# Optimization experiments

Hardware: AMD Instinct MI355X
Metric: run time of the kernel (lower is better)

Reference implementation:

```python
import jax, jax.numpy as jnp
import numpy as np

B, D, E, H, L = 32768, 512, 10, 128, 2  # batch, input_dim, max_charts, expert hidden, latent_dim
RH1, RH2 = 256, 128                      # router hidden sizes
TAU = 3.0


def setup_inputs() -> dict:
    key = jax.random.key(0)
    ks = jax.random.split(key, 16)
    rnd = lambda k, *s: (jax.random.normal(k, s, jnp.float32) * 0.05)
    return {
        "x": jax.random.normal(ks[0], (B, D), jnp.float32),
        "u": jax.random.uniform(ks[1], (B, E), jnp.float32),
        # router params (last layer init ~ N(0, 0.01), bias 0, as in _init_router)
        "rw1": rnd(ks[2], D, RH1), "rb1": jnp.zeros((RH1,), jnp.float32),
        "rw2": rnd(ks[3], RH1, RH2), "rb2": jnp.zeros((RH2,), jnp.float32),
        "rw3": jax.random.normal(ks[4], (RH2, E), jnp.float32) * 0.01,
        "rb3": jnp.zeros((E,), jnp.float32),
        # stacked expert params: all 10 experts batched along leading dim
        "ew1": rnd(ks[5], E, D, H), "eb1": rnd(ks[6], E, H),
        "ew2": rnd(ks[7], E, H, H), "eb2": rnd(ks[8], E, H),
        "ew3": rnd(ks[9], E, H, L), "eb3": rnd(ks[10], E, L),
    }


def reference(x, u, rw1, rb1, rw2, rb2, rw3, rb3, ew1, eb1, ew2, eb2, ew3, eb3):
    # router MLP: D -> 256 -> 128 -> E
    h = jax.nn.relu(x @ rw1 + rb1)
    h = jax.nn.relu(h @ rw2 + rb2)
    logits = h @ rw3 + rb3                                  # [B, E]
    # gumbel_softmax(tau=3.0, hard=False): softmax((logits + gumbel)/tau)
    g = -jnp.log(-jnp.log(jnp.clip(u, 1e-10, 1.0)) + 1e-10)
    weights = jax.nn.softmax((logits + g) / TAU, axis=1)    # [B, E]
    # all 10 experts as batched GEMMs (fuses the python loop over charts)
    h1 = jax.nn.relu(jnp.einsum('bi,eio->beo', x, ew1) + eb1[None])   # [B, E, H]
    h2 = jax.nn.relu(jnp.einsum('beh,eho->beo', h1, ew2) + eb2[None]) # [B, E, H]
    zc = jnp.einsum('beh,ehl->bel', h2, ew3) + eb3[None]              # [B, E, L]
    z = jnp.einsum('be,bel->bl', weights, zc)                         # [B, L]
    chart_outputs = jnp.transpose(zc, (1, 0, 2))                      # [E, B, L]
    return z, weights, chart_outputs
```

## Files before the change

### kernel.cpp

```cpp
#include <hip/hip_runtime.h>
#include <stdint.h>

typedef __bf16 bf16x8 __attribute__((ext_vector_type(8)));
typedef float floatx4 __attribute__((ext_vector_type(4)));
typedef unsigned short ushort_t;

__device__ __forceinline__ ushort_t bf16rne(float f) {
    union { float f; unsigned u; } v; v.f = f;
    return (ushort_t)((v.u + 0x7fffu + ((v.u >> 16) & 1u)) >> 16);
}

__device__ __forceinline__ void gl_lds16(const ushort_t* g, ushort_t* l) {
    __builtin_amdgcn_global_load_lds(
        (const __attribute__((address_space(1))) unsigned int*)g,
        (__attribute__((address_space(3))) unsigned int*)l, 16, 0, 0);
}

__device__ __forceinline__ void transpose_body(const float* __restrict__ in,
                                               ushort_t* __restrict__ outp,
                                               int idx, int K, int N, int total) {
    if (idx >= total) return;
    int kn = K * N;
    int e = idx / kn;
    int r = idx - e * kn;
    int n = r / K;
    int k = r - n * K;
    outp[idx] = bf16rne(in[e * kn + k * N + n]);
}

__global__ void prep(const float* __restrict__ x, ushort_t* __restrict__ x16,
                     const float* __restrict__ ew1, ushort_t* __restrict__ ew1t,
                     const float* __restrict__ ew2, ushort_t* __restrict__ ew2t,
                     const float* __restrict__ rw1, ushort_t* __restrict__ rw1t,
                     const float* __restrict__ rw2, ushort_t* __restrict__ rw2t) {
    int b = blockIdx.x, tid = threadIdx.x;
    if (b < 16384) {
        int i = b * 256 + tid;
        float4 f = ((const float4*)x)[i];
        union { ushort_t s[4]; uint2 v; } pk;
        pk.s[0] = bf16rne(f.x); pk.s[1] = bf16rne(f.y);
        pk.s[2] = bf16rne(f.z); pk.s[3] = bf16rne(f.w);
        ((uint2*)x16)[i] = pk.v;
    } else if (b < 18944) {
        transpose_body(ew1, ew1t, (b - 16384) * 256 + tid, 512, 128, 655360);
    } else if (b < 19584) {
        transpose_body(ew2, ew2t, (b - 18944) * 256 + tid, 128, 128, 163840);
    } else if (b < 20096) {
        transpose_body(rw1, rw1t, (b - 19584) * 256 + tid, 512, 256, 131072);
    } else {
        transpose_body(rw2, rw2t, (b - 20096) * 256 + tid, 256, 128, 32768);
    }
}

__global__ __launch_bounds__(256, 4)
void router_l1(const ushort_t* __restrict__ x16, const ushort_t* __restrict__ rw1t,
               const float* __restrict__ rb1, ushort_t* __restrict__ hr1) {
    __shared__ alignas(16) ushort_t sX[4096];
    __shared__ alignas(16) ushort_t sW[4096];
    __shared__ float sBias[128];

    const int tid = threadIdx.x;
    const int rb = blockIdx.x, nb = blockIdx.y;
    const int wave = tid >> 6, lane = tid & 63;
    const int ln15 = lane & 15, q = lane >> 4;
    const int wm = (wave & 1) * 64, wn = (wave >> 1) * 64;
    const int mhalf = wm >> 6, nhalf = wn >> 6;

    if (tid < 128) sBias[tid] = rb1[nb * 128 + tid];

    const ushort_t* xblk = x16 + (size_t)rb * 128 * 512;
    const ushort_t* wbase = rw1t + (size_t)nb * 128 * 512;

    const int s0 = wave, s1 = wave + 4;
    const int srow0 = (wave * 16) + (lane >> 2);
    const int srow1 = 64 + (wave * 16) + (lane >> 2);
    const int scol = (lane & 3) * 8;

    floatx4 acc[4][4];
#pragma unroll
    for (int i = 0; i < 4; ++i)
#pragma unroll
        for (int j = 0; j < 4; ++j) acc[i][j] = (floatx4){0.f, 0.f, 0.f, 0.f};

    for (int k0 = 0; k0 < 512; k0 += 32) {
        __syncthreads();
        gl_lds16(xblk + (size_t)srow0 * 512 + k0 + scol, &sX[s0 * 512]);
        gl_lds16(xblk + (size_t)srow1 * 512 + k0 + scol, &sX[s1 * 512]);
        gl_lds16(wbase + (size_t)srow0 * 512 + k0 + scol, &sW[s0 * 512]);
        gl_lds16(wbase + (size_t)srow1 * 512 + k0 + scol, &sW[s1 * 512]);
        __syncthreads();
        bf16x8 a[4], b[4];
#pragma unroll
        for (int t = 0; t < 4; ++t) a[t] = *(const bf16x8*)(&sW[(mhalf * 4 + t) * 512 + ln15 * 32 + q * 8]);
#pragma unroll
        for (int t = 0; t < 4; ++t) b[t] = *(const bf16x8*)(&sX[(nhalf * 4 + t) * 512 + ln15 * 32 + q * 8]);
#pragma unroll
        for (int i = 0; i < 4; ++i)
#pragma unroll
            for (int j = 0; j < 4; ++j)
                acc[i][j] = __builtin_amdgcn_mfma_f32_16x16x32_bf16(a[i], b[j], acc[i][j], 0, 0, 0);
    }

    const int rbase = rb * 128;
#pragma unroll
    for (int i = 0; i < 4; ++i) {
        int n0 = wm + i * 16 + q * 4;
#pragma unroll
        for (int j = 0; j < 4; ++j) {
            int row = wn + j * 16 + ln15;
            union { ushort_t s[4]; uint2 v; } pk;
#pragma unroll
            for (int r = 0; r < 4; ++r)
                pk.s[r] = bf16rne(fmaxf(acc[i][j][r] + sBias[n0 + r], 0.f));
            *(uint2*)(&hr1[(size_t)(rbase + row) * 256 + nb * 128 + n0]) = pk.v;
        }
    }
}

__global__ __launch_bounds__(256, 2)
void router2(const ushort_t* __restrict__ hr1, const ushort_t* __restrict__ rw2t,
             const float* __restrict__ rb2, const float* __restrict__ rw3,
             const float* __restrict__ rb3, const float* __restrict__ u,
             float* __restrict__ wts, float* __restrict__ z) {
    __shared__ alignas(16) ushort_t sA[4096];
    __shared__ alignas(16) ushort_t sB[4096];
    __shared__ float sw3[1280];
    __shared__ float sBias[128];
    __shared__ float lgbuf[128][10];

    const int tid = threadIdx.x;
    const int rb = blockIdx.x;
    const int wave = tid >> 6, lane = tid & 63;
    const int ln15 = lane & 15, q = lane >> 4;
    const int wm = (wave & 1) * 64, wn = (wave >> 1) * 64;
    const int mhalf = wm >> 6, nhalf = wn >> 6;

    for (int i = tid; i < 1280; i += 256) sw3[i] = rw3[i];
    if (tid < 128) sBias[tid] = rb2[tid];

    const ushort_t* brow = hr1 + (size_t)rb * 128 * 256;
    const int s0 = wave, s1 = wave + 4;
    const int srow0 = (wave * 16) + (lane >> 2);
    const int srow1 = 64 + (wave * 16) + (lane >> 2);
    const int scol = (lane & 3) * 8;

    floatx4 acc2[4][4];
#pragma unroll
    for (int i = 0; i < 4; ++i)
#pragma unroll
        for (int j = 0; j < 4; ++j) acc2[i][j] = (floatx4){0.f, 0.f, 0.f, 0.f};

    for (int k0 = 0; k0 < 256; k0 += 32) {
        __syncthreads();
        gl_lds16(rw2t + (size_t)srow0 * 256 + k0 + scol, &sA[s0 * 512]);
        gl_lds16(rw2t + (size_t)srow1 * 256 + k0 + scol, &sA[s1 * 512]);
        gl_lds16(brow + (size_t)srow0 * 256 + k0 + scol, &sB[s0 * 512]);
        gl_lds16(brow + (size_t)srow1 * 256 + k0 + scol, &sB[s1 * 512]);
        __syncthreads();
        bf16x8 a[4], b[4];
#pragma unroll
        for (int t = 0; t < 4; ++t) a[t] = *(const bf16x8*)(&sA[(mhalf * 4 + t) * 512 + ln15 * 32 + q * 8]);
#pragma unroll
        for (int t = 0; t < 4; ++t) b[t] = *(const bf16x8*)(&sB[(nhalf * 4 + t) * 512 + ln15 * 32 + q * 8]);
#pragma unroll
        for (int i = 0; i < 4; ++i)
#pragma unroll
            for (int j = 0; j < 4; ++j)
                acc2[i][j] = __builtin_amdgcn_mfma_f32_16x16x32_bf16(a[i], b[j], acc2[i][j], 0, 0, 0);
    }

    float lg[4][10];
#pragma unroll
    for (int j = 0; j < 4; ++j)
#pragma unroll
        for (int ee = 0; ee < 10; ++ee) lg[j][ee] = 0.f;
#pragma unroll
    for (int i = 0; i < 4; ++i) {
#pragma unroll
        for (int r = 0; r < 4; ++r) {
            int n = wm + i * 16 + q * 4 + r;
            float bias = sBias[n];
            const float* w3r = &sw3[n * 10];
#pragma unroll
            for (int j = 0; j < 4; ++j) {
                float val = fmaxf(acc2[i][j][r] + bias, 0.f);
#pragma unroll
                for (int ee = 0; ee < 10; ++ee) lg[j][ee] += val * w3r[ee];
            }
        }
    }
#pragma unroll
    for (int j = 0; j < 4; ++j)
#pragma unroll
        for (int ee = 0; ee < 10; ++ee) {
            lg[j][ee] += __shfl_xor(lg[j][ee], 16, 64);
            lg[j][ee] += __shfl_xor(lg[j][ee], 32, 64);
        }
    if (wm == 0 && q == 0) {
#pragma unroll
        for (int j = 0; j < 4; ++j) {
            int row = wn + 16 * j + ln15;
#pragma unroll
            for (int ee = 0; ee < 10; ++ee) lgbuf[row][ee] = lg[j][ee];
        }
    }
    __syncthreads();
    if (wm == 64 && q == 0) {
#pragma unroll
        for (int j = 0; j < 4; ++j) {
            int row = wn + 16 * j + ln15;
#pragma unroll
            for (int ee = 0; ee < 10; ++ee) lgbuf[row][ee] += lg[j][ee];
        }
    }
    __syncthreads();
    if (tid < 128) {
        int grow = rb * 128 + tid;
        float v[10], mx = -1e30f;
#pragma unroll
        for (int ee = 0; ee < 10; ++ee) {
            float uu = u[(size_t)grow * 10 + ee];
            uu = fminf(fmaxf(uu, 1e-10f), 1.0f);
            float g = -logf(-logf(uu) + 1e-10f);
            v[ee] = (lgbuf[tid][ee] + rb3[ee] + g) * (1.0f / 3.0f);
            mx = fmaxf(mx, v[ee]);
        }
        float s = 0.f;
#pragma unroll
        for (int ee = 0; ee < 10; ++ee) { v[ee] = expf(v[ee] - mx); s += v[ee]; }
        float inv = 1.0f / s;
#pragma unroll
        for (int ee = 0; ee < 10; ++ee) wts[(size_t)grow * 10 + ee] = v[ee] * inv;
    }
    z[rb * 256 + tid] = 0.f;
}

__global__ __launch_bounds__(256, 3)
void expert_fused(const ushort_t* __restrict__ x16, const ushort_t* __restrict__ ew1t,
                  const ushort_t* __restrict__ ew2t, const float* __restrict__ eb1,
                  const float* __restrict__ eb2, const float* __restrict__ ew3,
                  const float* __restrict__ eb3, const float* __restrict__ wts,
                  float* __restrict__ chart, float* __restrict__ z) {
    __shared__ alignas(16) ushort_t sX[4096];
    __shared__ alignas(16) ushort_t sW[4096];
    __shared__ alignas(16) ushort_t sH1[16384];
    __shared__ float sB1[128];
    __shared__ float sB2[128];
    __shared__ float sW3[256];
    __shared__ float zbuf[128][2];

    const int tid = threadIdx.x;
    const int id = blockIdx.x;
    const int xcd = id & 7, local = id >> 3;
    const int e = local % 10;
    const int rb = xcd * 32 + local / 10;

    const int wave = tid >> 6, lane = tid & 63;
    const int ln15 = lane & 15, q = lane >> 4;
    const int wm = (wave & 1) * 64, wn = (wave >> 1) * 64;
    const int mhalf = wm >> 6, nhalf = wn >> 6;

    if (tid < 128) sB1[tid] = eb1[e * 128 + tid];
    else sB2[tid - 128] = eb2[e * 128 + (tid - 128)];
    sW3[tid] = ew3[e * 256 + tid];

    const ushort_t* xblk = x16 + (size_t)rb * 128 * 512;
    const ushort_t* w1 = ew1t + (size_t)e * 128 * 512;
    const ushort_t* w2 = ew2t + (size_t)e * 128 * 128;

    const int s0 = wave, s1 = wave + 4;
    const int srow0 = (wave * 16) + (lane >> 2);
    const int srow1 = 64 + (wave * 16) + (lane >> 2);
    const int scol = (lane & 3) * 8;

    {
        floatx4 acc[4][4];
#pragma unroll
        for (int i = 0; i < 4; ++i)
#pragma unroll
            for (int j = 0; j < 4; ++j) acc[i][j] = (floatx4){0.f, 0.f, 0.f, 0.f};

        for (int k0 = 0; k0 < 512; k0 += 32) {
            __syncthreads();
            gl_lds16(xblk + (size_t)srow0 * 512 + k0 + scol, &sX[s0 * 512]);
            gl_lds16(xblk + (size_t)srow1 * 512 + k0 + scol, &sX[s1 * 512]);
            gl_lds16(w1 + (size_t)srow0 * 512 + k0 + scol, &sW[s0 * 512]);
            gl_lds16(w1 + (size_t)srow1 * 512 + k0 + scol, &sW[s1 * 512]);
            __syncthreads();
            bf16x8 a[4], b[4];
#pragma unroll
            for (int t = 0; t < 4; ++t) a[t] = *(const bf16x8*)(&sW[(mhalf * 4 + t) * 512 + ln15 * 32 + q * 8]);
#pragma unroll
            for (int t = 0; t < 4; ++t) b[t] = *(const bf16x8*)(&sX[(nhalf * 4 + t) * 512 + ln15 * 32 + q * 8]);
#pragma unroll
            for (int i = 0; i < 4; ++i)
#pragma unroll
                for (int j = 0; j < 4; ++j)
                    acc[i][j] = __builtin_amdgcn_mfma_f32_16x16x32_bf16(a[i], b[j], acc[i][j], 0, 0, 0);
        }

#pragma unroll
        for (int i = 0; i < 4; ++i) {
            int ks = mhalf * 2 + (i >> 1);
            int hlow = 16 * (i & 1) + 4 * q;
            int h0 = wm + i * 16 + q * 4;
#pragma unroll
            for (int j = 0; j < 4; ++j) {
                union { ushort_t s[4]; uint2 v; } pk;
#pragma unroll
                for (int r = 0; r < 4; ++r)
                    pk.s[r] = bf16rne(fmaxf(acc[i][j][r] + sB1[h0 + r], 0.f));
                *(uint2*)(&sH1[nhalf * 8192 + ks * 2048 + j * 512 + ln15 * 32 + hlow]) = pk.v;
            }
        }
    }

    floatx4 acc2[4][4];
#pragma unroll
    for (int i = 0; i < 4; ++i)
#pragma unroll
        for (int j = 0; j < 4; ++j) acc2[i][j] = (floatx4){0.f, 0.f, 0.f, 0.f};

    for (int k0 = 0; k0 < 128; k0 += 32) {
        __syncthreads();
        gl_lds16(w2 + (size_t)srow0 * 128 + k0 + scol, &sW[s0 * 512]);
        gl_lds16(w2 + (size_t)srow1 * 128 + k0 + scol, &sW[s1 * 512]);
        __syncthreads();
        bf16x8 a[4], b[4];
#pragma unroll
        for (int t = 0; t < 4; ++t) a[t] = *(const bf16x8*)(&sW[(mhalf * 4 + t) * 512 + ln15 * 32 + q * 8]);
#pragma unroll
        for (int t = 0; t < 4; ++t) b[t] = *(const bf16x8*)(&sH1[nhalf * 8192 + (k0 >> 5) * 2048 + t * 512 + ln15 * 32 + q * 8]);
#pragma unroll
        for (int i = 0; i < 4; ++i)
#pragma unroll
            for (int j = 0; j < 4; ++j)
                acc2[i][j] = __builtin_amdgcn_mfma_f32_16x16x32_bf16(a[i], b[j], acc2[i][j], 0, 0, 0);
    }

    float zc0[4] = {0.f, 0.f, 0.f, 0.f}, zc1[4] = {0.f, 0.f, 0.f, 0.f};
#pragma unroll
    for (int i = 0; i < 4; ++i) {
        int o0 = wm + i * 16 + q * 4;
#pragma unroll
        for (int r = 0; r < 4; ++r) {
            int o = o0 + r;
            float w3a = sW3[2 * o], w3b = sW3[2 * o + 1];
            float bias = sB2[o];
#pragma unroll
            for (int j = 0; j < 4; ++j) {
                float val = fmaxf(acc2[i][j][r] + bias, 0.f);
                zc0[j] += val * w3a;
                zc1[j] += val * w3b;
            }
        }
    }
#pragma unroll
    for (int j = 0; j < 4; ++j) {
        zc0[j] += __shfl_xor(zc0[j], 16, 64);
        zc0[j] += __shfl_xor(zc0[j], 32, 64);
        zc1[j] += __shfl_xor(zc1[j], 16, 64);
        zc1[j] += __shfl_xor(zc1[j], 32, 64);
    }
    if (wm == 0 && q == 0) {
#pragma unroll
        for (int j = 0; j < 4; ++j) {
            int row = wn + j * 16 + ln15;
            zbuf[row][0] = zc0[j];
            zbuf[row][1] = zc1[j];
        }
    }
    __syncthreads();
    if (wm == 64 && q == 0) {
#pragma unroll
        for (int j = 0; j < 4; ++j) {
            int row = wn + j * 16 + ln15;
            zbuf[row][0] += zc0[j];
            zbuf[row][1] += zc1[j];
        }
    }
    __syncthreads();
    {
        int row = tid >> 1, l = tid & 1;
        int grow = rb * 128 + row;
        float vz = zbuf[row][l] + eb3[e * 2 + l];
        chart[(size_t)e * 65536 + (size_t)grow * 2 + l] = vz;
        atomicAdd(&z[(size_t)grow * 2 + l], wts[(size_t)grow * 10 + e] * vz);
    }
}

extern "C" void kernel_launch(void* const* d_in, const int* in_sizes, int n_in,
                              void* d_out, int out_size, void* d_ws, size_t ws_size,
                              hipStream_t stream) {
    const float* x = (const float*)d_in[0];
    const float* u = (const float*)d_in[1];
    const float* rw1 = (const float*)d_in[2];
    const float* rb1 = (const float*)d_in[3];
    const float* rw2 = (const float*)d_in[4];
    const float* rb2 = (const float*)d_in[5];
    const float* rw3 = (const float*)d_in[6];
    const float* rb3 = (const float*)d_in[7];
    const float* ew1 = (const float*)d_in[8];
    const float* eb1 = (const float*)d_in[9];
    const float* ew2 = (const float*)d_in[10];
    const float* eb2 = (const float*)d_in[11];
    const float* ew3 = (const float*)d_in[12];
    const float* eb3 = (const float*)d_in[13];
    float* out = (float*)d_out;
    float* z = out;
    float* wts = out + 65536;
    float* chart = out + 393216;

    ushort_t* x16  = (ushort_t*)d_ws;
    ushort_t* ew1t = x16 + 16777216;
    ushort_t* ew2t = ew1t + 655360;
    ushort_t* rw1t = ew2t + 163840;
    ushort_t* rw2t = rw1t + 131072;
    ushort_t* hr1  = rw2t + 32768;

    prep<<<20224, 256, 0, stream>>>(x, x16, ew1, ew1t, ew2, ew2t, rw1, rw1t, rw2, rw2t);

    router_l1<<<dim3(256, 2), 256, 0, stream>>>(x16, rw1t, rb1, hr1);
    router2<<<256, 256, 0, stream>>>(hr1, rw2t, rb2, rw3, rb3, u, wts, z);

    expert_fused<<<2560, 256, 0, stream>>>(x16, ew1t, ew2t, eb1, eb2, ew3, eb3,
                                           wts, chart, z);
}
```

Before: 228.6 us.

## Reorder LDS tile layout for conflict-free MFMA operand reads, halve W2 staging syncs

Changes the shared-memory tile layout in all three GEMM kernels so each lane's 16-byte fragment sits at a contiguous lane*8 offset. The global-to-LDS loads map lane&15 to row and lane>>4 to the k-chunk to match. This is meant to remove LDS bank conflicts on the bf16x8 operand reads feeding the MFMAs, and the expert H1 scratch layout is rewritten to the same scheme. The second expert layer now stages two k-slices of W2 per barrier pair instead of one, cutting the number of __syncthreads. The global load pattern changes from 4 lanes per row to 16 rows by 4 chunks, which may reduce per-row coalescing.

```diff
diff --git a/kernel.cpp b/kernel.cpp
--- a/kernel.cpp
+++ b/kernel.cpp
@@ -52,11 +52,11 @@
     }
 }
 
+
 __global__ __launch_bounds__(256, 4)
 void router_l1(const ushort_t* __restrict__ x16, const ushort_t* __restrict__ rw1t,
                const float* __restrict__ rb1, ushort_t* __restrict__ hr1) {
-    __shared__ alignas(16) ushort_t sX[4096];
-    __shared__ alignas(16) ushort_t sW[4096];
+    __shared__ alignas(16) ushort_t sXW[8192];
     __shared__ float sBias[128];
 
     const int tid = threadIdx.x;
@@ -71,10 +71,9 @@
     const ushort_t* xblk = x16 + (size_t)rb * 128 * 512;
     const ushort_t* wbase = rw1t + (size_t)nb * 128 * 512;
 
-    const int s0 = wave, s1 = wave + 4;
-    const int srow0 = (wave * 16) + (lane >> 2);
-    const int srow1 = 64 + (wave * 16) + (lane >> 2);
-    const int scol = (lane & 3) * 8;
+    const int srow = lane & 15;
+    const int scol = (lane >> 4) * 8;
+    const int rg0 = wave * 2, rg1 = wave * 2 + 1;
 
     floatx4 acc[4][4];
 #pragma unroll
@@ -84,16 +83,16 @@
 
     for (int k0 = 0; k0 < 512; k0 += 32) {
         __syncthreads();
-        gl_lds16(xblk + (size_t)srow0 * 512 + k0 + scol, &sX[s0 * 512]);
-        gl_lds16(xblk + (size_t)srow1 * 512 + k0 + scol, &sX[s1 * 512]);
-        gl_lds16(wbase + (size_t)srow0 * 512 + k0 + scol, &sW[s0 * 512]);
-        gl_lds16(wbase + (size_t)srow1 * 512 + k0 + scol, &sW[s1 * 512]);
+        gl_lds16(xblk + (size_t)(rg0 * 16 + srow) * 512 + k0 + scol, &sXW[rg0 * 512]);
+        gl_lds16(xblk + (size_t)(rg1 * 16 + srow) * 512 + k0 + scol, &sXW[rg1 * 512]);
+        gl_lds16(wbase + (size_t)(rg0 * 16 + srow) * 512 + k0 + scol, &sXW[4096 + rg0 * 512]);
+        gl_lds16(wbase + (size_t)(rg1 * 16 + srow) * 512 + k0 + scol, &sXW[4096 + rg1 * 512]);
         __syncthreads();
         bf16x8 a[4], b[4];
 #pragma unroll
-        for (int t = 0; t < 4; ++t) a[t] = *(const bf16x8*)(&sW[(mhalf * 4 + t) * 512 + ln15 * 32 + q * 8]);
-#pragma unroll
-        for (int t = 0; t < 4; ++t) b[t] = *(const bf16x8*)(&sX[(nhalf * 4 + t) * 512 + ln15 * 32 + q * 8]);
+        for (int t = 0; t < 4; ++t) a[t] = *(const bf16x8*)(&sXW[4096 + (mhalf * 4 + t) * 512 + lane * 8]);
+#pragma unroll
+        for (int t = 0; t < 4; ++t) b[t] = *(const bf16x8*)(&sXW[(nhalf * 4 + t) * 512 + lane * 8]);
 #pragma unroll
         for (int i = 0; i < 4; ++i)
 #pragma unroll
@@ -122,8 +121,7 @@
              const float* __restrict__ rb2, const float* __restrict__ rw3,
              const float* __restrict__ rb3, const float* __restrict__ u,
              float* __restrict__ wts, float* __restrict__ z) {
-    __shared__ alignas(16) ushort_t sA[4096];
-    __shared__ alignas(16) ushort_t sB[4096];
+    __shared__ alignas(16) ushort_t sXW[8192];
     __shared__ float sw3[1280];
     __shared__ float sBias[128];
     __shared__ float lgbuf[128][10];
@@ -139,10 +137,9 @@
     if (tid < 128) sBias[tid] = rb2[tid];
 
     const ushort_t* brow = hr1 + (size_t)rb * 128 * 256;
-    const int s0 = wave, s1 = wave + 4;
-    const int srow0 = (wave * 16) + (lane >> 2);
-    const int srow1 = 64 + (wave * 16) + (lane >> 2);
-    const int scol = (lane & 3) * 8;
+    const int srow = lane & 15;
+    const int scol = (lane >> 4) * 8;
+    const int rg0 = wave * 2, rg1 = wave * 2 + 1;
 
     floatx4 acc2[4][4];
 #pragma unroll
@@ -152,16 +149,16 @@
 
     for (int k0 = 0; k0 < 256; k0 += 32) {
         __syncthreads();
-        gl_lds16(rw2t + (size_t)srow0 * 256 + k0 + scol, &sA[s0 * 512]);
-        gl_lds16(rw2t + (size_t)srow1 * 256 + k0 + scol, &sA[s1 * 512]);
-        gl_lds16(brow + (size_t)srow0 * 256 + k0 + scol, &sB[s0 * 512]);
-        gl_lds16(brow + (size_t)srow1 * 256 + k0 + scol, &sB[s1 * 512]);
+        gl_lds16(brow + (size_t)(rg0 * 16 + srow) * 256 + k0 + scol, &sXW[rg0 * 512]);
+        gl_lds16(brow + (size_t)(rg1 * 16 + srow) * 256 + k0 + scol, &sXW[rg1 * 512]);
+        gl_lds16(rw2t + (size_t)(rg0 * 16 + srow) * 256 + k0 + scol, &sXW[4096 + rg0 * 512]);
+        gl_lds16(rw2t + (size_t)(rg1 * 16 + srow) * 256 + k0 + scol, &sXW[4096 + rg1 * 512]);
         __syncthreads();
         bf16x8 a[4], b[4];
 #pragma unroll
-        for (int t = 0; t < 4; ++t) a[t] = *(const bf16x8*)(&sA[(mhalf * 4 + t) * 512 + ln15 * 32 + q * 8]);
-#pragma unroll
-        for (int t = 0; t < 4; ++t) b[t] = *(const bf16x8*)(&sB[(nhalf * 4 + t) * 512 + ln15 * 32 + q * 8]);
+        for (int t = 0; t < 4; ++t) a[t] = *(const bf16x8*)(&sXW[4096 + (mhalf * 4 + t) * 512 + lane * 8]);
+#pragma unroll
+        for (int t = 0; t < 4; ++t) b[t] = *(const bf16x8*)(&sXW[(nhalf * 4 + t) * 512 + lane * 8]);
 #pragma unroll
         for (int i = 0; i < 4; ++i)
 #pragma unroll
@@ -241,8 +238,7 @@
                   const float* __restrict__ eb2, const float* __restrict__ ew3,
                   const float* __restrict__ eb3, const float* __restrict__ wts,
                   float* __restrict__ chart, float* __restrict__ z) {
-    __shared__ alignas(16) ushort_t sX[4096];
-    __shared__ alignas(16) ushort_t sW[4096];
+    __shared__ alignas(16) ushort_t sXW[8192];
     __shared__ alignas(16) ushort_t sH1[16384];
     __shared__ float sB1[128];
     __shared__ float sB2[128];
@@ -268,10 +264,9 @@
     const ushort_t* w1 = ew1t + (size_t)e * 128 * 512;
     const ushort_t* w2 = ew2t + (size_t)e * 128 * 128;
 
-    const int s0 = wave, s1 = wave + 4;
-    const int srow0 = (wave * 16) + (lane >> 2);
-    const int srow1 = 64 + (wave * 16) + (lane >> 2);
-    const int scol = (lane & 3) * 8;
+    const int srow = lane & 15;
+    const int scol = (lane >> 4) * 8;
+    const int rg0 = wave * 2, rg1 = wave * 2 + 1;
 
     {
         floatx4 acc[4][4];
@@ -282,16 +277,16 @@
 
         for (int k0 = 0; k0 < 512; k0 += 32) {
             __syncthreads();
-            gl_lds16(xblk + (size_t)srow0 * 512 + k0 + scol, &sX[s0 * 512]);
-            gl_lds16(xblk + (size_t)srow1 * 512 + k0 + scol, &sX[s1 * 512]);
-            gl_lds16(w1 + (size_t)srow0 * 512 + k0 + scol, &sW[s0 * 512]);
-            gl_lds16(w1 + (size_t)srow1 * 512 + k0 + scol, &sW[s1 * 512]);
+            gl_lds16(xblk + (size_t)(rg0 * 16 + srow) * 512 + k0 + scol, &sXW[rg0 * 512]);
+            gl_lds16(xblk + (size_t)(rg1 * 16 + srow) * 512 + k0 + scol, &sXW[rg1 * 512]);
+            gl_lds16(w1 + (size_t)(rg0 * 16 + srow) * 512 + k0 + scol, &sXW[4096 + rg0 * 512]);
+            gl_lds16(w1 + (size_t)(rg1 * 16 + srow) * 512 + k0 + scol, &sXW[4096 + rg1 * 512]);
             __syncthreads();
             bf16x8 a[4], b[4];
 #pragma unroll
-            for (int t = 0; t < 4; ++t) a[t] = *(const bf16x8*)(&sW[(mhalf * 4 + t) * 512 + ln15 * 32 + q * 8]);
-#pragma unroll
-            for (int t = 0; t < 4; ++t) b[t] = *(const bf16x8*)(&sX[(nhalf * 4 + t) * 512 + ln15 * 32 + q * 8]);
+            for (int t = 0; t < 4; ++t) a[t] = *(const bf16x8*)(&sXW[4096 + (mhalf * 4 + t) * 512 + lane * 8]);
+#pragma unroll
+            for (int t = 0; t < 4; ++t) b[t] = *(const bf16x8*)(&sXW[(nhalf * 4 + t) * 512 + lane * 8]);
 #pragma unroll
             for (int i = 0; i < 4; ++i)
 #pragma unroll
@@ -301,16 +296,18 @@
 
 #pragma unroll
         for (int i = 0; i < 4; ++i) {
-            int ks = mhalf * 2 + (i >> 1);
-            int hlow = 16 * (i & 1) + 4 * q;
-            int h0 = wm + i * 16 + q * 4;
+            int hbase = wm + 16 * i;
+            int kh = hbase >> 5;
+            int qhi = (hbase >> 4) & 1;
+            int slotq = 2 * qhi + (q >> 1);
+            int h0 = hbase + q * 4;
 #pragma unroll
             for (int j = 0; j < 4; ++j) {
                 union { ushort_t s[4]; uint2 v; } pk;
 #pragma unroll
                 for (int r = 0; r < 4; ++r)
                     pk.s[r] = bf16rne(fmaxf(acc[i][j][r] + sB1[h0 + r], 0.f));
-                *(uint2*)(&sH1[nhalf * 8192 + ks * 2048 + j * 512 + ln15 * 32 + hlow]) = pk.v;
+                *(uint2*)(&sH1[kh * 4096 + (nhalf * 4 + j) * 512 + slotq * 128 + ln15 * 8 + (q & 1) * 4]) = pk.v;
             }
         }
     }
@@ -321,21 +318,30 @@
 #pragma unroll
         for (int j = 0; j < 4; ++j) acc2[i][j] = (floatx4){0.f, 0.f, 0.f, 0.f};
 
-    for (int k0 = 0; k0 < 128; k0 += 32) {
-        __syncthreads();
-        gl_lds16(w2 + (size_t)srow0 * 128 + k0 + scol, &sW[s0 * 512]);
-        gl_lds16(w2 + (size_t)srow1 * 128 + k0 + scol, &sW[s1 * 512]);
-        __syncthreads();
-        bf16x8 a[4], b[4];
-#pragma unroll
-        for (int t = 0; t < 4; ++t) a[t] = *(const bf16x8*)(&sW[(mhalf * 4 + t) * 512 + ln15 * 32 + q * 8]);
-#pragma unroll
-        for (int t = 0; t < 4; ++t) b[t] = *(const bf16x8*)(&sH1[nhalf * 8192 + (k0 >> 5) * 2048 + t * 512 + ln15 * 32 + q * 8]);
-#pragma unroll
-        for (int i = 0; i < 4; ++i)
-#pragma unroll
-            for (int j = 0; j < 4; ++j)
-                acc2[i][j] = __builtin_amdgcn_mfma_f32_16x16x32_bf16(a[i], b[j], acc2[i][j], 0, 0, 0);
+    for (int p = 0; p < 2; ++p) {
+        __syncthreads();
+#pragma unroll
+        for (int r = 0; r < 4; ++r) {
+            int s = wave * 4 + r;
+            int khl = s >> 3, rg = s & 7;
+            int kh = p * 2 + khl;
+            gl_lds16(w2 + (size_t)(rg * 16 + srow) * 128 + kh * 32 + scol, &sXW[s * 512]);
+        }
+        __syncthreads();
+#pragma unroll
+        for (int khl = 0; khl < 2; ++khl) {
+            int kh = p * 2 + khl;
+            bf16x8 a[4], b[4];
+#pragma unroll
+            for (int t = 0; t < 4; ++t) a[t] = *(const bf16x8*)(&sXW[(khl * 8 + mhalf * 4 + t) * 512 + lane * 8]);
+#pragma unroll
+            for (int t = 0; t < 4; ++t) b[t] = *(const bf16x8*)(&sH1[kh * 4096 + (nhalf * 4 + t) * 512 + lane * 8]);
+#pragma unroll
+            for (int i = 0; i < 4; ++i)
+#pragma unroll
+                for (int j = 0; j < 4; ++j)
+                    acc2[i][j] = __builtin_amdgcn_mfma_f32_16x16x32_bf16(a[i], b[j], acc2[i][j], 0, 0, 0);
+        }
     }
 
     float zc0[4] = {0.f, 0.f, 0.f, 0.f}, zc1[4] = {0.f, 0.f, 0.f, 0.f};
```

Measured after the change: 259.7 us. 13.6% more time.
